# Kernel tuning notes

Measured on AMD Instinct MI355X. Metric: run time of the kernel, lower is better.

Reference implementation:

```python
import jax, jax.numpy as jnp
import numpy as np

C_IN = 256
RED = 8
C_QK = C_IN // RED  # 32


def setup_inputs() -> dict:
    key = jax.random.key(0)
    ks = jax.random.split(key, 7)
    B, C, H, W = 4, C_IN, 64, 64
    s = 1.0 / np.sqrt(C)
    return {
        "x": jax.random.normal(ks[0], (B, C, H, W), dtype=jnp.float32),
        "wq": jax.random.uniform(ks[1], (C_QK, C), jnp.float32, -s, s),
        "bq": jax.random.uniform(ks[2], (C_QK,), jnp.float32, -s, s),
        "wk": jax.random.uniform(ks[3], (C_QK, C), jnp.float32, -s, s),
        "bk": jax.random.uniform(ks[4], (C_QK,), jnp.float32, -s, s),
        "wv": jax.random.uniform(ks[5], (C, C), jnp.float32, -s, s),
        "bv": jax.random.uniform(ks[6], (C,), jnp.float32, -s, s),
        "gamma": jnp.zeros((1,), dtype=jnp.float32),
    }


def reference(x, wq, bq, wk, bk, wv, bv, gamma):
    B, C, H, W = x.shape
    N = H * W
    xf = x.reshape(B, C, N)  # flatten spatial tokens
    # 1x1 convs == per-pixel linear projections over channels
    q = jnp.einsum("oc,bcn->bno", wq, xf) + bq            # (B, N, C_qk)
    k = jnp.einsum("oc,bcn->bon", wk, xf) + bk[:, None]   # (B, C_qk, N)
    v = jnp.einsum("oc,bcn->bon", wv, xf) + bv[:, None]   # (B, C, N)
    # unscaled attention: softmax over keys (last dim)
    attn = jax.nn.softmax(jnp.einsum("bio,boj->bij", q, k), axis=-1)  # (B, N, N)
    # attended[b,c,i] = sum_j v[b,c,j] * attn[b,i,j]  (bmm with attn^T)
    attended = jnp.einsum("bcj,bij->bci", v, attn).reshape(B, C, H, W)
    output = gamma[0] * attended + x
    attention_map = attn.mean(axis=1).reshape(B, H, W)
    return output, attention_map
```

## Files before the change

### kernel.cpp

```cpp
#include <hip/hip_runtime.h>


#define B_   4
#define C_   256
#define N_   4096
#define CQK_ 32
#define BCN_ (B_*C_*N_)
#define BN_  (B_*N_)
#define TP_  68

typedef __attribute__((ext_vector_type(8))) short short8v;
typedef __attribute__((ext_vector_type(4))) float f32x4;
typedef unsigned short ushort_t;

__device__ __forceinline__ ushort_t f2bf(float f) {
  unsigned u = __builtin_bit_cast(unsigned, f);
  u += 0x7FFFu + ((u >> 16) & 1u);
  return (ushort_t)(u >> 16);
}
__device__ __forceinline__ float bf2f(ushort_t h) {
  unsigned u = ((unsigned)h) << 16;
  return __builtin_bit_cast(float, u);
}
__device__ __forceinline__ short8v ld8f(const float* p) {
  float4 a = *(const float4*)p, b = *(const float4*)(p + 4);
  short8v r;
  r[0]=f2bf(a.x); r[1]=f2bf(a.y); r[2]=f2bf(a.z); r[3]=f2bf(a.w);
  r[4]=f2bf(b.x); r[5]=f2bf(b.y); r[6]=f2bf(b.z); r[7]=f2bf(b.w);
  return r;
}

__global__ __launch_bounds__(256) void
k_prep(const float* __restrict__ x, float* __restrict__ out,
       float* __restrict__ l, ushort_t* __restrict__ xbt) {
  __shared__ ushort_t tile[64 * TP_];
  int blk = blockIdx.x, tid = threadIdx.x;
  int b = blk >> 8, cg = (blk >> 6) & 3, ng = blk & 63;
  int c0 = cg << 6, n0 = ng << 6;
  const float* xb = x + ((size_t)b * C_ + c0) * N_ + n0;
  float* ob = out + ((size_t)b * C_ + c0) * N_ + n0;
#pragma unroll
  for (int it = 0; it < 4; ++it) {
    int flat4 = it * 256 + tid;
    int r = flat4 >> 4, c4 = flat4 & 15;
    float4 v = *(const float4*)(xb + (size_t)r * N_ + c4 * 4);
    *(float4*)(ob + (size_t)r * N_ + c4 * 4) = v;
    ushort4 h;
    h.x = f2bf(v.x); h.y = f2bf(v.y); h.z = f2bf(v.z); h.w = f2bf(v.w);
    *(ushort4*)(&tile[r * TP_ + c4 * 4]) = h;
  }
  __syncthreads();
#pragma unroll
  for (int it = 0; it < 4; ++it) {
    int flat4 = it * 256 + tid;
    int nr = flat4 >> 4, cc4 = flat4 & 15;
    ushort4 h;
    h.x = tile[(cc4 * 4 + 0) * TP_ + nr];
    h.y = tile[(cc4 * 4 + 1) * TP_ + nr];
    h.z = tile[(cc4 * 4 + 2) * TP_ + nr];
    h.w = tile[(cc4 * 4 + 3) * TP_ + nr];
    *(ushort4*)(xbt + ((size_t)(b * N_) + n0 + nr) * C_ + c0 + cc4 * 4) = h;
  }
  if (blk < 64) {
    int idx = blk * 256 + tid;
    l[idx] = 0.0f;
    out[BCN_ + idx] = 0.0f;
  }
}

__global__ __launch_bounds__(256) void
k_projqk(const ushort_t* __restrict__ xbt,
         const float* __restrict__ wq, const float* __restrict__ bq,
         const float* __restrict__ wk, const float* __restrict__ bk,
         const float* __restrict__ wv, const float* __restrict__ bv,
         const float* __restrict__ gamma,
         ushort_t* __restrict__ qb, ushort_t* __restrict__ kb,
         float* __restrict__ v_t) {
  int blk = blockIdx.x;
  int b = blk >> 8, ng = blk & 255;
  int wave = threadIdx.x >> 6, lane = threadIdx.x & 63;
  int col16 = lane & 15, quad = lane >> 4;
  int mt = wave;
  bool isq = mt < 2;
  int co_row = (mt & 1) * 16 + col16;
  const float* wrow = (isq ? wq : wk) + co_row * C_;
  int n = ng * 16 + col16;
  const ushort_t* xrow = xbt + ((size_t)(b * N_) + n) * C_;

  short8v bfr[8];
#pragma unroll
  for (int ks = 0; ks < 8; ++ks)
    bfr[ks] = *(const short8v*)(xrow + ks * 32 + quad * 8);

  f32x4 c = {0.f, 0.f, 0.f, 0.f};
#pragma unroll
  for (int ks = 0; ks < 8; ++ks) {
    short8v afr = ld8f(wrow + ks * 32 + quad * 8);
    c = __builtin_amdgcn_mfma_f32_16x16x32_bf16(afr, bfr[ks], c, 0, 0, 0);
  }
  int co_base = (mt & 1) * 16 + quad * 4;
  const float* bias = isq ? bq : bk;
  ushort4 pk;
  pk.x = f2bf(c[0] + bias[co_base + 0]); pk.y = f2bf(c[1] + bias[co_base + 1]);
  pk.z = f2bf(c[2] + bias[co_base + 2]); pk.w = f2bf(c[3] + bias[co_base + 3]);
  ushort_t* dst = isq ? qb : kb;
  *(ushort4*)(dst + ((size_t)(b * N_) + n) * CQK_ + co_base) = pk;

  if (gamma[0] != 0.0f) {
    for (int m2 = wave * 4; m2 < wave * 4 + 4; ++m2) {
      f32x4 cv = {0.f, 0.f, 0.f, 0.f};
      const float* wvr = wv + (m2 * 16 + col16) * C_;
#pragma unroll
      for (int ks = 0; ks < 8; ++ks) {
        short8v afr = ld8f(wvr + ks * 32 + quad * 8);
        cv = __builtin_amdgcn_mfma_f32_16x16x32_bf16(afr, bfr[ks], cv, 0, 0, 0);
      }
      int co = m2 * 16 + quad * 4;
      float4 o;
      o.x = cv[0] + bv[co];     o.y = cv[1] + bv[co + 1];
      o.z = cv[2] + bv[co + 2]; o.w = cv[3] + bv[co + 3];
      *(float4*)(v_t + ((size_t)(b * N_) + n) * C_ + co) = o;
    }
  }
}

__global__ __launch_bounds__(256) void
k_rowsA(const ushort_t* __restrict__ qb, const ushort_t* __restrict__ kb,
        float* __restrict__ l) {
  int blk = blockIdx.x;
  int b = blk >> 8, rg = (blk >> 2) & 63, js = blk & 3;
  int wave = threadIdx.x >> 6, lane = threadIdx.x & 63;
  int col16 = lane & 15, quad = lane >> 4;
  const ushort_t* qbb = qb + (size_t)b * N_ * CQK_;
  const ushort_t* kbb = kb + (size_t)b * N_ * CQK_;
  int i_base = rg * 64;
  short8v a[4];
#pragma unroll
  for (int t = 0; t < 4; ++t)
    a[t] = *(const short8v*)(qbb + (i_base + t * 16 + col16) * CQK_ + quad * 8);
  float racc[16];
#pragma unroll
  for (int r = 0; r < 16; ++r) racc[r] = 0.0f;
  int j_base = js * 1024 + wave * 256;
#pragma unroll 4
  for (int t = 0; t < 16; ++t) {
    short8v bfr = *(const short8v*)(kbb + (j_base + t * 16 + col16) * CQK_ + quad * 8);
#pragma unroll
    for (int m = 0; m < 4; ++m) {
      f32x4 c = {0.f, 0.f, 0.f, 0.f};
      c = __builtin_amdgcn_mfma_f32_16x16x32_bf16(a[m], bfr, c, 0, 0, 0);
      racc[m * 4 + 0] += __expf(c[0]); racc[m * 4 + 1] += __expf(c[1]);
      racc[m * 4 + 2] += __expf(c[2]); racc[m * 4 + 3] += __expf(c[3]);
    }
  }
#pragma unroll
  for (int r = 0; r < 16; ++r) {
    float v = racc[r];
    v += __shfl_xor(v, 1); v += __shfl_xor(v, 2);
    v += __shfl_xor(v, 4); v += __shfl_xor(v, 8);
    racc[r] = v;
  }
  if (col16 == 0) {
    float* lb = l + b * N_ + i_base;
#pragma unroll
    for (int m = 0; m < 4; ++m)
#pragma unroll
      for (int rr = 0; rr < 4; ++rr)
        atomicAdd(&lb[m * 16 + quad * 4 + rr], racc[m * 4 + rr]);
  }
}

__global__ __launch_bounds__(256) void
k_mapB(const ushort_t* __restrict__ qb, const ushort_t* __restrict__ kb,
       const float* __restrict__ l, float* __restrict__ map) {
  int blk = blockIdx.x;
  int b = blk >> 8, jg = (blk >> 4) & 15, isp = blk & 15;
  int wave = threadIdx.x >> 6, lane = threadIdx.x & 63;
  int col16 = lane & 15, quad = lane >> 4;
  const ushort_t* qbb = qb + (size_t)b * N_ * CQK_;
  const ushort_t* kbb = kb + (size_t)b * N_ * CQK_;
  int j_base = jg * 256 + wave * 64;
  short8v a[4];
#pragma unroll
  for (int t = 0; t < 4; ++t)
    a[t] = *(const short8v*)(kbb + (j_base + t * 16 + col16) * CQK_ + quad * 8);
  float csum[16];
#pragma unroll
  for (int r = 0; r < 16; ++r) csum[r] = 0.0f;
  int i_base = isp * 256;
#pragma unroll 4
  for (int t = 0; t < 16; ++t) {
    int i0 = i_base + t * 16;
    short8v bfr = *(const short8v*)(qbb + (i0 + col16) * CQK_ + quad * 8);
    float winv = 1.0f / l[b * N_ + i0 + col16];
#pragma unroll
    for (int m = 0; m < 4; ++m) {
      f32x4 c = {0.f, 0.f, 0.f, 0.f};
      c = __builtin_amdgcn_mfma_f32_16x16x32_bf16(a[m], bfr, c, 0, 0, 0);
      csum[m * 4 + 0] += __expf(c[0]) * winv; csum[m * 4 + 1] += __expf(c[1]) * winv;
      csum[m * 4 + 2] += __expf(c[2]) * winv; csum[m * 4 + 3] += __expf(c[3]) * winv;
    }
  }
#pragma unroll
  for (int r = 0; r < 16; ++r) {
    float v = csum[r];
    v += __shfl_xor(v, 1); v += __shfl_xor(v, 2);
    v += __shfl_xor(v, 4); v += __shfl_xor(v, 8);
    csum[r] = v;
  }
  if (col16 == 0) {
    float* mp = map + b * N_ + j_base;
#pragma unroll
    for (int m = 0; m < 4; ++m)
#pragma unroll
      for (int rr = 0; rr < 4; ++rr)
        atomicAdd(&mp[m * 16 + quad * 4 + rr], csum[m * 4 + rr] * (1.0f / (float)N_));
  }
}

__global__ __launch_bounds__(256) void
k_pv(const ushort_t* __restrict__ qb, const ushort_t* __restrict__ kb,
     const float* __restrict__ v_t, const float* __restrict__ l,
     const float* __restrict__ gamma, float* __restrict__ out) {
  if (gamma[0] == 0.0f) return;
  __shared__ float qs[32 * CQK_];
  __shared__ float invl[32];
  __shared__ float ps[32 * 256];
  int blk = blockIdx.x;
  int b = blk >> 9, i0 = ((blk >> 2) & 127) << 5, jsp = blk & 3;
  int tid = threadIdx.x;
  for (int r = tid; r < 32 * CQK_; r += 256)
    qs[r] = bf2f(qb[((size_t)(b * N_) + i0) * CQK_ + r]);
  if (tid < 32) invl[tid] = 1.0f / l[b * N_ + i0 + tid];
  __syncthreads();
  float g = gamma[0];
  float acc[32];
#pragma unroll
  for (int i = 0; i < 32; ++i) acc[i] = 0.0f;
  for (int jt = jsp * 4; jt < jsp * 4 + 4; ++jt) {
    int j = jt * 256 + tid;
    const ushort_t* krow = kb + ((size_t)(b * N_) + j) * CQK_;
    float kcol[CQK_];
#pragma unroll
    for (int o = 0; o < CQK_; ++o) kcol[o] = bf2f(krow[o]);
#pragma unroll
    for (int i = 0; i < 32; ++i) {
      float s = 0.0f;
#pragma unroll
      for (int o = 0; o < CQK_; ++o) s += qs[i * CQK_ + o] * kcol[o];
      ps[i * 256 + tid] = __expf(s) * invl[i];
    }
    __syncthreads();
    const float* vtb = v_t + ((size_t)(b * N_) + jt * 256) * C_;
    for (int jj = 0; jj < 256; ++jj) {
      float vv = vtb[(size_t)jj * C_ + tid];
#pragma unroll
      for (int i = 0; i < 32; ++i) acc[i] += ps[i * 256 + jj] * vv;
    }
    __syncthreads();
  }
  float* ob = out + ((size_t)(b * C_) + tid) * N_ + i0;
#pragma unroll
  for (int i = 0; i < 32; ++i) atomicAdd(&ob[i], g * acc[i]);
}

extern "C" void kernel_launch(void* const* d_in, const int* in_sizes, int n_in,
                              void* d_out, int out_size, void* d_ws, size_t ws_size,
                              hipStream_t stream) {
  const float* x     = (const float*)d_in[0];
  const float* wq    = (const float*)d_in[1];
  const float* bq    = (const float*)d_in[2];
  const float* wk    = (const float*)d_in[3];
  const float* bk    = (const float*)d_in[4];
  const float* wv    = (const float*)d_in[5];
  const float* bv    = (const float*)d_in[6];
  const float* gamma = (const float*)d_in[7];
  float* out = (float*)d_out;
  float* wsf = (float*)d_ws;
  float*    l    = wsf;
  ushort_t* xbt  = (ushort_t*)(wsf + 16384);
  ushort_t* qb   = (ushort_t*)(wsf + 2113536);
  ushort_t* kb   = (ushort_t*)(wsf + 2375680);
  float*    v_t  = wsf + 2637824;

  k_prep  <<<1024, 256, 0, stream>>>(x, out, l, xbt);
  k_projqk<<<1024, 256, 0, stream>>>(xbt, wq, bq, wk, bk, wv, bv, gamma, qb, kb, v_t);
  k_rowsA <<<1024, 256, 0, stream>>>(qb, kb, l);
  k_mapB  <<<1024, 256, 0, stream>>>(qb, kb, l, out + BCN_);
  k_pv    <<<2048, 256, 0, stream>>>(qb, kb, v_t, l, gamma, out);
}
```

Measured before the change: 133.4 us.

## Fuse bf16 transpose prep into QK projection and switch softmax to exp2

Merges the x copy/bf16 transpose kernel with the Q/K/V projection kernel, staging the transposed bf16 tile in LDS instead of writing and rereading a global xbt buffer, and removes one launch. Q is prescaled by log2(e) so the softmax kernels can use the hardware exp2 instruction. In the map kernel the row normaliser is folded in as -log2(l), used as the MFMA accumulator init, which replaces a per-element multiply. The exchange is half as many blocks in the fused kernel (512) and a larger LDS tile, plus some extra rounding from folding the log2(e) scale into the bf16 Q.

```diff
diff --git a/kernel.cpp b/kernel.cpp
--- a/kernel.cpp
+++ b/kernel.cpp
@@ -7,9 +7,11 @@
 #define CQK_ 32
 #define BCN_ (B_*C_*N_)
 #define BN_  (B_*N_)
-#define TP_  68
+#define TP_  260
+#define LOG2E 1.4426950408889634f
 
 typedef __attribute__((ext_vector_type(8))) short short8v;
+typedef __attribute__((ext_vector_type(4))) short short4v;
 typedef __attribute__((ext_vector_type(4))) float f32x4;
 typedef unsigned short ushort_t;
 
@@ -29,96 +31,93 @@
   r[4]=f2bf(b.x); r[5]=f2bf(b.y); r[6]=f2bf(b.z); r[7]=f2bf(b.w);
   return r;
 }
-
-__global__ __launch_bounds__(256) void
-k_prep(const float* __restrict__ x, float* __restrict__ out,
-       float* __restrict__ l, ushort_t* __restrict__ xbt) {
-  __shared__ ushort_t tile[64 * TP_];
+__device__ __forceinline__ short8v ld8lds(const ushort_t* p) {
+  short4v lo = *(const short4v*)p, hi = *(const short4v*)(p + 4);
+  return __builtin_shufflevector(lo, hi, 0, 1, 2, 3, 4, 5, 6, 7);
+}
+
+__global__ __launch_bounds__(256) void
+k_prep(const float* __restrict__ x,
+       const float* __restrict__ wq, const float* __restrict__ bq,
+       const float* __restrict__ wk, const float* __restrict__ bk,
+       const float* __restrict__ wv, const float* __restrict__ bv,
+       const float* __restrict__ gamma,
+       float* __restrict__ out, float* __restrict__ l,
+       ushort_t* __restrict__ qb, ushort_t* __restrict__ kb,
+       float* __restrict__ v_t) {
+  __shared__ ushort_t xs[32 * TP_];
   int blk = blockIdx.x, tid = threadIdx.x;
-  int b = blk >> 8, cg = (blk >> 6) & 3, ng = blk & 63;
-  int c0 = cg << 6, n0 = ng << 6;
-  const float* xb = x + ((size_t)b * C_ + c0) * N_ + n0;
-  float* ob = out + ((size_t)b * C_ + c0) * N_ + n0;
-#pragma unroll
-  for (int it = 0; it < 4; ++it) {
-    int flat4 = it * 256 + tid;
-    int r = flat4 >> 4, c4 = flat4 & 15;
-    float4 v = *(const float4*)(xb + (size_t)r * N_ + c4 * 4);
-    *(float4*)(ob + (size_t)r * N_ + c4 * 4) = v;
-    ushort4 h;
-    h.x = f2bf(v.x); h.y = f2bf(v.y); h.z = f2bf(v.z); h.w = f2bf(v.w);
-    *(ushort4*)(&tile[r * TP_ + c4 * 4]) = h;
-  }
-  __syncthreads();
-#pragma unroll
-  for (int it = 0; it < 4; ++it) {
-    int flat4 = it * 256 + tid;
-    int nr = flat4 >> 4, cc4 = flat4 & 15;
-    ushort4 h;
-    h.x = tile[(cc4 * 4 + 0) * TP_ + nr];
-    h.y = tile[(cc4 * 4 + 1) * TP_ + nr];
-    h.z = tile[(cc4 * 4 + 2) * TP_ + nr];
-    h.w = tile[(cc4 * 4 + 3) * TP_ + nr];
-    *(ushort4*)(xbt + ((size_t)(b * N_) + n0 + nr) * C_ + c0 + cc4 * 4) = h;
+  int b = blk >> 7, n0 = (blk & 127) << 5;
+#pragma unroll
+  for (int it = 0; it < 8; ++it) {
+    int flat = it * 256 + tid;
+    int c = flat >> 3, t4 = flat & 7;
+    size_t off = ((size_t)(b * C_) + c) * N_ + n0 + t4 * 4;
+    float4 v = *(const float4*)(x + off);
+    *(float4*)(out + off) = v;
+    ushort_t* dst = &xs[(t4 * 4) * TP_ + c];
+    dst[0]        = f2bf(v.x);
+    dst[TP_]      = f2bf(v.y);
+    dst[2 * TP_]  = f2bf(v.z);
+    dst[3 * TP_]  = f2bf(v.w);
   }
   if (blk < 64) {
     int idx = blk * 256 + tid;
     l[idx] = 0.0f;
     out[BCN_ + idx] = 0.0f;
   }
-}
-
-__global__ __launch_bounds__(256) void
-k_projqk(const ushort_t* __restrict__ xbt,
-         const float* __restrict__ wq, const float* __restrict__ bq,
-         const float* __restrict__ wk, const float* __restrict__ bk,
-         const float* __restrict__ wv, const float* __restrict__ bv,
-         const float* __restrict__ gamma,
-         ushort_t* __restrict__ qb, ushort_t* __restrict__ kb,
-         float* __restrict__ v_t) {
-  int blk = blockIdx.x;
-  int b = blk >> 8, ng = blk & 255;
-  int wave = threadIdx.x >> 6, lane = threadIdx.x & 63;
+  __syncthreads();
+
+  int wave = tid >> 6, lane = tid & 63;
   int col16 = lane & 15, quad = lane >> 4;
-  int mt = wave;
-  bool isq = mt < 2;
-  int co_row = (mt & 1) * 16 + col16;
-  const float* wrow = (isq ? wq : wk) + co_row * C_;
-  int n = ng * 16 + col16;
-  const ushort_t* xrow = xbt + ((size_t)(b * N_) + n) * C_;
-
+  int g = wave & 1;
+  bool isq = wave < 2;
+  int tok_l = g * 16 + col16;
+  int n = n0 + tok_l;
   short8v bfr[8];
 #pragma unroll
   for (int ks = 0; ks < 8; ++ks)
-    bfr[ks] = *(const short8v*)(xrow + ks * 32 + quad * 8);
-
-  f32x4 c = {0.f, 0.f, 0.f, 0.f};
-#pragma unroll
-  for (int ks = 0; ks < 8; ++ks) {
-    short8v afr = ld8f(wrow + ks * 32 + quad * 8);
-    c = __builtin_amdgcn_mfma_f32_16x16x32_bf16(afr, bfr[ks], c, 0, 0, 0);
-  }
-  int co_base = (mt & 1) * 16 + quad * 4;
+    bfr[ks] = ld8lds(&xs[tok_l * TP_ + ks * 32 + quad * 8]);
+
+  const float* wrow = isq ? wq : wk;
   const float* bias = isq ? bq : bk;
-  ushort4 pk;
-  pk.x = f2bf(c[0] + bias[co_base + 0]); pk.y = f2bf(c[1] + bias[co_base + 1]);
-  pk.z = f2bf(c[2] + bias[co_base + 2]); pk.w = f2bf(c[3] + bias[co_base + 3]);
   ushort_t* dst = isq ? qb : kb;
-  *(ushort4*)(dst + ((size_t)(b * N_) + n) * CQK_ + co_base) = pk;
+#pragma unroll
+  for (int mt = 0; mt < 2; ++mt) {
+    f32x4 c = {0.f, 0.f, 0.f, 0.f};
+#pragma unroll
+    for (int ks = 0; ks < 8; ++ks) {
+      short8v afr = ld8f(wrow + (mt * 16 + col16) * C_ + ks * 32 + quad * 8);
+      c = __builtin_amdgcn_mfma_f32_16x16x32_bf16(afr, bfr[ks], c, 0, 0, 0);
+    }
+    int co = mt * 16 + quad * 4;
+    ushort4 pk;
+    if (isq) {
+      pk.x = f2bf((c[0] + bias[co + 0]) * LOG2E);
+      pk.y = f2bf((c[1] + bias[co + 1]) * LOG2E);
+      pk.z = f2bf((c[2] + bias[co + 2]) * LOG2E);
+      pk.w = f2bf((c[3] + bias[co + 3]) * LOG2E);
+    } else {
+      pk.x = f2bf(c[0] + bias[co + 0]); pk.y = f2bf(c[1] + bias[co + 1]);
+      pk.z = f2bf(c[2] + bias[co + 2]); pk.w = f2bf(c[3] + bias[co + 3]);
+    }
+    *(ushort4*)(dst + ((size_t)(b * N_) + n) * CQK_ + co) = pk;
+  }
 
   if (gamma[0] != 0.0f) {
-    for (int m2 = wave * 4; m2 < wave * 4 + 4; ++m2) {
-      f32x4 cv = {0.f, 0.f, 0.f, 0.f};
-      const float* wvr = wv + (m2 * 16 + col16) * C_;
+    int half = wave >> 1;
+    for (int vt = 0; vt < 8; ++vt) {
+      int tile = half * 8 + vt;
+      f32x4 c = {0.f, 0.f, 0.f, 0.f};
 #pragma unroll
       for (int ks = 0; ks < 8; ++ks) {
-        short8v afr = ld8f(wvr + ks * 32 + quad * 8);
-        cv = __builtin_amdgcn_mfma_f32_16x16x32_bf16(afr, bfr[ks], cv, 0, 0, 0);
+        short8v afr = ld8f(wv + (tile * 16 + col16) * C_ + ks * 32 + quad * 8);
+        c = __builtin_amdgcn_mfma_f32_16x16x32_bf16(afr, bfr[ks], c, 0, 0, 0);
       }
-      int co = m2 * 16 + quad * 4;
+      int co = tile * 16 + quad * 4;
       float4 o;
-      o.x = cv[0] + bv[co];     o.y = cv[1] + bv[co + 1];
-      o.z = cv[2] + bv[co + 2]; o.w = cv[3] + bv[co + 3];
+      o.x = c[0] + bv[co];     o.y = c[1] + bv[co + 1];
+      o.z = c[2] + bv[co + 2]; o.w = c[3] + bv[co + 3];
       *(float4*)(v_t + ((size_t)(b * N_) + n) * C_ + co) = o;
     }
   }
@@ -149,8 +148,10 @@
     for (int m = 0; m < 4; ++m) {
       f32x4 c = {0.f, 0.f, 0.f, 0.f};
       c = __builtin_amdgcn_mfma_f32_16x16x32_bf16(a[m], bfr, c, 0, 0, 0);
-      racc[m * 4 + 0] += __expf(c[0]); racc[m * 4 + 1] += __expf(c[1]);
-      racc[m * 4 + 2] += __expf(c[2]); racc[m * 4 + 3] += __expf(c[3]);
+      racc[m * 4 + 0] += __builtin_amdgcn_exp2f(c[0]);
+      racc[m * 4 + 1] += __builtin_amdgcn_exp2f(c[1]);
+      racc[m * 4 + 2] += __builtin_amdgcn_exp2f(c[2]);
+      racc[m * 4 + 3] += __builtin_amdgcn_exp2f(c[3]);
     }
   }
 #pragma unroll
@@ -192,13 +193,15 @@
   for (int t = 0; t < 16; ++t) {
     int i0 = i_base + t * 16;
     short8v bfr = *(const short8v*)(qbb + (i0 + col16) * CQK_ + quad * 8);
-    float winv = 1.0f / l[b * N_ + i0 + col16];
+    float llog = -__builtin_amdgcn_logf(l[b * N_ + i0 + col16]);
+    f32x4 cinit = {llog, llog, llog, llog};
 #pragma unroll
     for (int m = 0; m < 4; ++m) {
-      f32x4 c = {0.f, 0.f, 0.f, 0.f};
-      c = __builtin_amdgcn_mfma_f32_16x16x32_bf16(a[m], bfr, c, 0, 0, 0);
-      csum[m * 4 + 0] += __expf(c[0]) * winv; csum[m * 4 + 1] += __expf(c[1]) * winv;
-      csum[m * 4 + 2] += __expf(c[2]) * winv; csum[m * 4 + 3] += __expf(c[3]) * winv;
+      f32x4 c = __builtin_amdgcn_mfma_f32_16x16x32_bf16(a[m], bfr, cinit, 0, 0, 0);
+      csum[m * 4 + 0] += __builtin_amdgcn_exp2f(c[0]);
+      csum[m * 4 + 1] += __builtin_amdgcn_exp2f(c[1]);
+      csum[m * 4 + 2] += __builtin_amdgcn_exp2f(c[2]);
+      csum[m * 4 + 3] += __builtin_amdgcn_exp2f(c[3]);
     }
   }
 #pragma unroll
@@ -248,7 +251,7 @@
       float s = 0.0f;
 #pragma unroll
       for (int o = 0; o < CQK_; ++o) s += qs[i * CQK_ + o] * kcol[o];
-      ps[i * 256 + tid] = __expf(s) * invl[i];
+      ps[i * 256 + tid] = __builtin_amdgcn_exp2f(s) * invl[i];
     }
     __syncthreads();
     const float* vtb = v_t + ((size_t)(b * N_) + jt * 256) * C_;
@@ -277,15 +280,14 @@
   const float* gamma = (const float*)d_in[7];
   float* out = (float*)d_out;
   float* wsf = (float*)d_ws;
-  float*    l    = wsf;
-  ushort_t* xbt  = (ushort_t*)(wsf + 16384);
-  ushort_t* qb   = (ushort_t*)(wsf + 2113536);
-  ushort_t* kb   = (ushort_t*)(wsf + 2375680);
-  float*    v_t  = wsf + 2637824;
-
-  k_prep  <<<1024, 256, 0, stream>>>(x, out, l, xbt);
-  k_projqk<<<1024, 256, 0, stream>>>(xbt, wq, bq, wk, bk, wv, bv, gamma, qb, kb, v_t);
-  k_rowsA <<<1024, 256, 0, stream>>>(qb, kb, l);
-  k_mapB  <<<1024, 256, 0, stream>>>(qb, kb, l, out + BCN_);
-  k_pv    <<<2048, 256, 0, stream>>>(qb, kb, v_t, l, gamma, out);
-}
+  float*    l   = wsf;
+  ushort_t* qb  = (ushort_t*)(wsf + 16384);
+  ushort_t* kb  = (ushort_t*)(wsf + 16384 + 262144);
+  float*    v_t = wsf + 16384 + 2 * 262144;
+
+  k_prep <<< 512, 256, 0, stream>>>(x, wq, bq, wk, bk, wv, bv, gamma,
+                                    out, l, qb, kb, v_t);
+  k_rowsA<<<1024, 256, 0, stream>>>(qb, kb, l);
+  k_mapB <<<1024, 256, 0, stream>>>(qb, kb, l, out + BCN_);
+  k_pv   <<<2048, 256, 0, stream>>>(qb, kb, v_t, l, gamma, out);
+}
```

Result: faster. 122.5 us (-8.2%).
